# Performance work log

Hardware: AMD Instinct MI355X
Metric: run time of the kernel (lower is better)

Reference implementation:

```python
import jax, jax.numpy as jnp
import numpy as np

NEG_INF = -1e30  # stand-in for -inf that is safe under fp16/bf16


def setup_inputs() -> dict:
    key = jax.random.key(0)
    k1, k2, k3, k4, k5 = jax.random.split(key, 5)
    B, NC, H, Wd = 32, 256, 64, 64
    MW, E = 32, 768
    images = jax.random.normal(k1, (B, NC, H, Wd), dtype=jnp.float32)
    words = jax.random.normal(k2, (B, MW, E), dtype=jnp.float32)
    # mask: True where word is ignored; ensure at least one word is attended per row
    mask = jax.random.randint(k3, (B, MW), 0, 2).astype(bool)
    mask = mask.at[:, 0].set(False)
    W = jax.random.normal(k4, (NC, E), dtype=jnp.float32) * (1.0 / np.sqrt(E))
    b = jax.random.normal(k5, (NC,), dtype=jnp.float32) * 0.01
    return {"images": images, "words": words, "mask": mask, "W": W, "b": b}


def reference(images, words, mask, W, b):
    B, NC, H, Wd = images.shape
    _, MW, E = words.shape
    # 1x1 conv over words == linear projection emb_dim -> nc_in
    # words_p: [B, nc_in, max_words]
    words_p = jnp.einsum('bme,ce->bcm', words, W) + b[None, :, None]
    # images flattened to pixels: [B, h*w, nc_in]
    imgs = images.reshape(B, NC, H * Wd).transpose(0, 2, 1)
    # attention scores: [B, h*w, max_words], scaled by 1/sqrt(nc_in)
    attn = jnp.einsum('bpc,bcm->bpm', imgs, words_p) * (1.0 / np.sqrt(NC))
    attn = jnp.where(mask[:, None, :], NEG_INF, attn)
    attn = jax.nn.softmax(attn, axis=-1)
    # weighted word sum per pixel: [B, nc_in, h*w]
    weighted = jnp.einsum('bcm,bpm->bcp', words_p, attn)
    weighted_words = weighted.reshape(B, NC, H, Wd)
    attn_out = attn.transpose(0, 2, 1).reshape(B, MW, H, Wd)
    return weighted_words, attn_out
```

## Files before the change

kernel.cpp:

```cpp
#include <hip/hip_runtime.h>
#include <math.h>

#define B_   32
#define NC_  256
#define HW_  4096
#define MW_  32
#define E_   768
#define NEG_BIG -3.0e38f

typedef float vf2 __attribute__((ext_vector_type(2)));
typedef float vf4 __attribute__((ext_vector_type(4)));

#define PART_OFF   0
#define WP_OFF     2097152
#define WT_OFF     2359296
#define WORDST_OFF 2555904
#define MASK_OFF   3342336

__global__ __launch_bounds__(256) void prep_kernel(
    const float* __restrict__ W, const float* __restrict__ words,
    const void* __restrict__ mask_raw,
    float* __restrict__ WT, float* __restrict__ wordsT,
    int* __restrict__ maskn) {
  const int tid = threadIdx.x;
  const int tx = tid & 31, ty = tid >> 5;
  if (blockIdx.x < 192) {
    __shared__ float t[32][33];
    const int tc = blockIdx.x / 24, te = blockIdx.x % 24;
    const int c0 = tc * 32, e0 = te * 32;
#pragma unroll
    for (int k = 0; k < 4; ++k) {
      const int r = ty + 8 * k;
      t[r][tx] = W[(c0 + r) * E_ + e0 + tx];
    }
    __syncthreads();
#pragma unroll
    for (int k = 0; k < 4; ++k) {
      const int r = ty + 8 * k;
      WT[(e0 + r) * NC_ + c0 + tx] = t[tx][r];
    }
  } else if (blockIdx.x < 960) {
    __shared__ float t[32][33];
    const int idx = blockIdx.x - 192;
    const int b = idx / 24, te = idx % 24;
    const int e0 = te * 32;
    const float* wsrc = words + (size_t)b * MW_ * E_;
    float* wdst = wordsT + (size_t)b * E_ * MW_;
#pragma unroll
    for (int k = 0; k < 4; ++k) {
      const int m = ty + 8 * k;
      t[m][tx] = wsrc[m * E_ + e0 + tx];
    }
    __syncthreads();
#pragma unroll
    for (int k = 0; k < 4; ++k) {
      const int e = ty + 8 * k;
      wdst[(e0 + e) * MW_ + tx] = t[tx][e];
    }
  } else {
    __shared__ int is_word;
    if (tid == 0) is_word = 1;
    __syncthreads();
    const int* mi = (const int*)mask_raw;
    const int v = mi[tid];
    if (v != 0 && v != 1 && v != 0x3F800000) is_word = 0;
    __syncthreads();
    if (is_word) {
#pragma unroll
      for (int j = 0; j < 4; ++j) { const int i = j * 256 + tid; maskn[i] = (mi[i] != 0); }
    } else {
      const unsigned char* mb = (const unsigned char*)mask_raw;
#pragma unroll
      for (int j = 0; j < 4; ++j) { const int i = j * 256 + tid; maskn[i] = (mb[i] != 0); }
    }
  }
}

__global__ __launch_bounds__(256) void stage1_partial(
    const float* __restrict__ wordsT, const float* __restrict__ WT,
    float* __restrict__ part) {
  const int c = threadIdx.x;
  const int b = blockIdx.x >> 3;
  const int chunk = blockIdx.x & 7;
  const int e0 = chunk * 96;
  const float* wt = wordsT + (size_t)b * E_ * MW_;
  float acc[32];
#pragma unroll
  for (int m = 0; m < 32; ++m) acc[m] = 0.f;
#pragma unroll 2
  for (int e = e0; e < e0 + 96; ++e) {
    const float wv = WT[(size_t)e * NC_ + c];
    const float* wr = wt + e * MW_;
#pragma unroll
    for (int m = 0; m < 32; ++m) acc[m] = fmaf(wv, wr[m], acc[m]);
  }
  float* pp = part + ((size_t)chunk * 32 + b) * 32 * 256;
#pragma unroll
  for (int m = 0; m < 32; ++m) pp[m * 256 + c] = acc[m];
}

__global__ __launch_bounds__(256) void stage1_reduce(
    const float* __restrict__ part, const float* __restrict__ bias,
    float* __restrict__ wp) {
  const int idx = blockIdx.x * 256 + threadIdx.x;
  const int c = idx & 255;
  const int m = (idx >> 8) & 31;
  const int b = idx >> 13;
  float s = bias[c];
#pragma unroll
  for (int k = 0; k < 8; ++k)
    s += part[(((size_t)k * 32 + b) * 32 + m) * 256 + c];
  wp[((size_t)b * 256 + c) * 32 + m] = s;
}

__global__ __launch_bounds__(128, 1) void attention_fused(
    const float* __restrict__ images, const float* __restrict__ wp,
    const int* __restrict__ maskn, float* __restrict__ out_w,
    float* __restrict__ out_a) {
  __shared__ float lwp[NC_ * MW_];
  const int tid = threadIdx.x;
  const int b = blockIdx.x & 31;
  const int po = ((blockIdx.x >> 5) << 7) + tid;
  const vf2* imgb = (const vf2*)(images + (size_t)b * NC_ * HW_);

  vf2 cur[16];
#pragma unroll
  for (int j = 0; j < 16; ++j)
    cur[j] = __builtin_nontemporal_load(&imgb[((size_t)j << 11) + po]);

  {
    const vf4* src = (const vf4*)(wp + (size_t)b * NC_ * MW_);
    vf4* dst = (vf4*)lwp;
#pragma unroll
    for (int k = 0; k < 16; ++k) dst[tid + (k << 7)] = src[tid + (k << 7)];
  }
  __syncthreads();

  float s0[32], s1[32];
#pragma unroll
  for (int m = 0; m < 32; ++m) { s0[m] = 0.f; s1[m] = 0.f; }

#pragma unroll 1
  for (int c0 = 0; c0 < 256; c0 += 16) {
    vf2 nxt[16];
    if (c0 + 16 < 256) {
#pragma unroll
      for (int j = 0; j < 16; ++j)
        nxt[j] = __builtin_nontemporal_load(&imgb[((size_t)(c0 + 16 + j) << 11) + po]);
    }
#pragma unroll
    for (int j = 0; j < 16; ++j) {
      const float* wrow = lwp + ((c0 + j) << 5);
      const vf2 v = cur[j];
#pragma unroll
      for (int m = 0; m < 32; ++m) {
        s0[m] = fmaf(v.x, wrow[m], s0[m]);
        s1[m] = fmaf(v.y, wrow[m], s1[m]);
      }
    }
#pragma unroll
    for (int j = 0; j < 16; ++j) cur[j] = nxt[j];
  }

  unsigned mbits = 0;
#pragma unroll
  for (int m = 0; m < 32; ++m)
    mbits |= (maskn[(b << 5) + m] != 0 ? 1u : 0u) << m;

  float mx0 = NEG_BIG, mx1 = NEG_BIG;
#pragma unroll
  for (int m = 0; m < 32; ++m) {
    s0[m] *= 0.0625f;
    s1[m] *= 0.0625f;
    if (!((mbits >> m) & 1u)) {
      mx0 = fmaxf(mx0, s0[m]);
      mx1 = fmaxf(mx1, s1[m]);
    }
  }
  float sum0 = 0.f, sum1 = 0.f;
#pragma unroll
  for (int m = 0; m < 32; ++m) {
    const bool msk = (mbits >> m) & 1u;
    const float e0 = msk ? 0.f : __expf(s0[m] - mx0);
    const float e1 = msk ? 0.f : __expf(s1[m] - mx1);
    s0[m] = e0; s1[m] = e1;
    sum0 += e0; sum1 += e1;
  }
  const float inv0 = 1.f / sum0, inv1 = 1.f / sum1;
  vf2* oa = (vf2*)out_a;
#pragma unroll
  for (int m = 0; m < 32; ++m) {
    s0[m] *= inv0;
    s1[m] *= inv1;
    vf2 a; a.x = s0[m]; a.y = s1[m];
    __builtin_nontemporal_store(a, &oa[((size_t)((b << 5) + m) << 11) + po]);
  }

  vf2* ow = (vf2*)out_w;
#pragma unroll 1
  for (int c0 = 0; c0 < 256; c0 += 8) {
#pragma unroll
    for (int jc = 0; jc < 8; ++jc) {
      const int c = c0 + jc;
      const float* wrow = lwp + (c << 5);
      float o0 = 0.f, o1 = 0.f;
#pragma unroll
      for (int m = 0; m < 32; ++m) {
        o0 = fmaf(wrow[m], s0[m], o0);
        o1 = fmaf(wrow[m], s1[m], o1);
      }
      vf2 o; o.x = o0; o.y = o1;
      __builtin_nontemporal_store(o, &ow[((size_t)((b << 8) + c) << 11) + po]);
    }
  }
}

extern "C" void kernel_launch(void* const* d_in, const int* in_sizes, int n_in,
                              void* d_out, int out_size, void* d_ws, size_t ws_size,
                              hipStream_t stream) {
  const float* images = (const float*)d_in[0];
  const float* words  = (const float*)d_in[1];
  const void*  mask   = d_in[2];
  const float* W      = (const float*)d_in[3];
  const float* bias   = (const float*)d_in[4];

  float* ws     = (float*)d_ws;
  float* part   = ws + PART_OFF;
  float* wp     = ws + WP_OFF;
  float* WT     = ws + WT_OFF;
  float* wordsT = ws + WORDST_OFF;
  int*   maskn  = (int*)(ws + MASK_OFF);

  float* out_w = (float*)d_out;
  float* out_a = out_w + (size_t)B_ * NC_ * HW_;

  prep_kernel<<<961, 256, 0, stream>>>(W, words, mask, WT, wordsT, maskn);
  stage1_partial<<<256, 256, 0, stream>>>(wordsT, WT, part);
  stage1_reduce<<<1024, 256, 0, stream>>>(part, bias, wp);
  attention_fused<<<512, 128, 0, stream>>>(images, wp, maskn, out_w, out_a);
}
```

Measured before the change: 308.3 us.

## Fuse stage1 reduction and mask decoding into attention kernel, double-buffer weight rows

Removes the stage1_reduce kernel and the mask-normalization block: each attention block now sums the 8 partial projections plus bias directly into shared memory and decodes the mask bits itself. The image prefetch depth drops from 16 to 8 channels, launch bounds no longer force 1 block per SM, and weight rows are double-buffered from LDS into registers for both GEMM loops. This saves a kernel launch and a global round-trip for wp, but every one of the 512 blocks now redundantly re-reduces the partials (16x duplicated reads per batch) and register pressure changes.

```diff
diff --git a/kernel.cpp b/kernel.cpp
--- a/kernel.cpp
+++ b/kernel.cpp
@@ -12,16 +12,12 @@
 typedef float vf4 __attribute__((ext_vector_type(4)));
 
 #define PART_OFF   0
-#define WP_OFF     2097152
 #define WT_OFF     2359296
 #define WORDST_OFF 2555904
-#define MASK_OFF   3342336
 
 __global__ __launch_bounds__(256) void prep_kernel(
     const float* __restrict__ W, const float* __restrict__ words,
-    const void* __restrict__ mask_raw,
-    float* __restrict__ WT, float* __restrict__ wordsT,
-    int* __restrict__ maskn) {
+    float* __restrict__ WT, float* __restrict__ wordsT) {
   const int tid = threadIdx.x;
   const int tx = tid & 31, ty = tid >> 5;
   if (blockIdx.x < 192) {
@@ -39,7 +35,7 @@
       const int r = ty + 8 * k;
       WT[(e0 + r) * NC_ + c0 + tx] = t[tx][r];
     }
-  } else if (blockIdx.x < 960) {
+  } else {
     __shared__ float t[32][33];
     const int idx = blockIdx.x - 192;
     const int b = idx / 24, te = idx % 24;
@@ -56,22 +52,6 @@
     for (int k = 0; k < 4; ++k) {
       const int e = ty + 8 * k;
       wdst[(e0 + e) * MW_ + tx] = t[tx][e];
-    }
-  } else {
-    __shared__ int is_word;
-    if (tid == 0) is_word = 1;
-    __syncthreads();
-    const int* mi = (const int*)mask_raw;
-    const int v = mi[tid];
-    if (v != 0 && v != 1 && v != 0x3F800000) is_word = 0;
-    __syncthreads();
-    if (is_word) {
-#pragma unroll
-      for (int j = 0; j < 4; ++j) { const int i = j * 256 + tid; maskn[i] = (mi[i] != 0); }
-    } else {
-      const unsigned char* mb = (const unsigned char*)mask_raw;
-#pragma unroll
-      for (int j = 0; j < 4; ++j) { const int i = j * 256 + tid; maskn[i] = (mb[i] != 0); }
     }
   }
 }
@@ -99,73 +79,118 @@
   for (int m = 0; m < 32; ++m) pp[m * 256 + c] = acc[m];
 }
 
-__global__ __launch_bounds__(256) void stage1_reduce(
-    const float* __restrict__ part, const float* __restrict__ bias,
-    float* __restrict__ wp) {
-  const int idx = blockIdx.x * 256 + threadIdx.x;
-  const int c = idx & 255;
-  const int m = (idx >> 8) & 31;
-  const int b = idx >> 13;
-  float s = bias[c];
-#pragma unroll
-  for (int k = 0; k < 8; ++k)
-    s += part[(((size_t)k * 32 + b) * 32 + m) * 256 + c];
-  wp[((size_t)b * 256 + c) * 32 + m] = s;
-}
-
-__global__ __launch_bounds__(128, 1) void attention_fused(
-    const float* __restrict__ images, const float* __restrict__ wp,
-    const int* __restrict__ maskn, float* __restrict__ out_w,
-    float* __restrict__ out_a) {
+__global__ __launch_bounds__(128) void attention_fused(
+    const float* __restrict__ images, const float* __restrict__ part,
+    const float* __restrict__ bias, const void* __restrict__ mask_raw,
+    float* __restrict__ out_w, float* __restrict__ out_a) {
   __shared__ float lwp[NC_ * MW_];
+  __shared__ int is_word;
   const int tid = threadIdx.x;
   const int b = blockIdx.x & 31;
   const int po = ((blockIdx.x >> 5) << 7) + tid;
   const vf2* imgb = (const vf2*)(images + (size_t)b * NC_ * HW_);
 
-  vf2 cur[16];
-#pragma unroll
-  for (int j = 0; j < 16; ++j)
+  if (tid == 0) is_word = 1;
+
+  vf2 cur[8];
+#pragma unroll
+  for (int j = 0; j < 8; ++j)
     cur[j] = __builtin_nontemporal_load(&imgb[((size_t)j << 11) + po]);
 
+#pragma unroll
+  for (int half = 0; half < 2; ++half) {
+    const int c = (half << 7) + tid;
+    const float bc = bias[c];
+    float row[32];
+#pragma unroll
+    for (int m = 0; m < 32; ++m) row[m] = bc;
+#pragma unroll
+    for (int k = 0; k < 8; ++k) {
+      const float* pk = part + (((size_t)k * 32 + b) * 32) * 256 + c;
+#pragma unroll
+      for (int m = 0; m < 32; ++m) row[m] += pk[(size_t)m * 256];
+    }
+    vf4* dst = (vf4*)(lwp + (c << 5));
+#pragma unroll
+    for (int q = 0; q < 8; ++q) {
+      vf4 t;
+      t.x = row[4 * q]; t.y = row[4 * q + 1];
+      t.z = row[4 * q + 2]; t.w = row[4 * q + 3];
+      dst[q] = t;
+    }
+  }
+  __syncthreads();
+
   {
-    const vf4* src = (const vf4*)(wp + (size_t)b * NC_ * MW_);
-    vf4* dst = (vf4*)lwp;
-#pragma unroll
-    for (int k = 0; k < 16; ++k) dst[tid + (k << 7)] = src[tid + (k << 7)];
+    const int* mi = (const int*)mask_raw;
+#pragma unroll
+    for (int q = 0; q < 2; ++q) {
+      const int v = mi[q * 128 + tid];
+      if (v != 0 && v != 1 && v != 0x3F800000) is_word = 0;
+    }
   }
   __syncthreads();
+  unsigned mbits = 0;
+  if (is_word) {
+    const int* mi = (const int*)mask_raw;
+#pragma unroll
+    for (int m = 0; m < 32; ++m)
+      mbits |= (mi[(b << 5) + m] != 0 ? 1u : 0u) << m;
+  } else {
+    const unsigned char* mb = (const unsigned char*)mask_raw;
+#pragma unroll
+    for (int m = 0; m < 32; ++m)
+      mbits |= (mb[(b << 5) + m] != 0 ? 1u : 0u) << m;
+  }
 
   float s0[32], s1[32];
 #pragma unroll
   for (int m = 0; m < 32; ++m) { s0[m] = 0.f; s1[m] = 0.f; }
 
+  vf4 wa[8], wb[8];
+#pragma unroll
+  for (int q = 0; q < 8; ++q) wa[q] = ((const vf4*)lwp)[q];
+
 #pragma unroll 1
-  for (int c0 = 0; c0 < 256; c0 += 16) {
-    vf2 nxt[16];
-    if (c0 + 16 < 256) {
-#pragma unroll
-      for (int j = 0; j < 16; ++j)
-        nxt[j] = __builtin_nontemporal_load(&imgb[((size_t)(c0 + 16 + j) << 11) + po]);
-    }
-#pragma unroll
-    for (int j = 0; j < 16; ++j) {
-      const float* wrow = lwp + ((c0 + j) << 5);
-      const vf2 v = cur[j];
-#pragma unroll
-      for (int m = 0; m < 32; ++m) {
-        s0[m] = fmaf(v.x, wrow[m], s0[m]);
-        s1[m] = fmaf(v.y, wrow[m], s1[m]);
+  for (int c0 = 0; c0 < 256; c0 += 8) {
+    vf2 nxt[8];
+    if (c0 + 8 < 256) {
+#pragma unroll
+      for (int j = 0; j < 8; ++j)
+        nxt[j] = __builtin_nontemporal_load(&imgb[((size_t)(c0 + 8 + j) << 11) + po]);
+    }
+#pragma unroll
+    for (int j = 0; j < 8; ++j) {
+      const int cn = c0 + j + 1;
+      if ((j & 1) == 0) {
+        if (cn < 256) {
+#pragma unroll
+          for (int q = 0; q < 8; ++q) wb[q] = ((const vf4*)lwp)[(cn << 3) + q];
+        }
+        const float* wr = (const float*)wa;
+        const vf2 v = cur[j];
+#pragma unroll
+        for (int m = 0; m < 32; ++m) {
+          s0[m] = fmaf(v.x, wr[m], s0[m]);
+          s1[m] = fmaf(v.y, wr[m], s1[m]);
+        }
+      } else {
+        if (cn < 256) {
+#pragma unroll
+          for (int q = 0; q < 8; ++q) wa[q] = ((const vf4*)lwp)[(cn << 3) + q];
+        }
+        const float* wr = (const float*)wb;
+        const vf2 v = cur[j];
+#pragma unroll
+        for (int m = 0; m < 32; ++m) {
+          s0[m] = fmaf(v.x, wr[m], s0[m]);
+          s1[m] = fmaf(v.y, wr[m], s1[m]);
+        }
       }
     }
 #pragma unroll
-    for (int j = 0; j < 16; ++j) cur[j] = nxt[j];
-  }
-
-  unsigned mbits = 0;
-#pragma unroll
-  for (int m = 0; m < 32; ++m)
-    mbits |= (maskn[(b << 5) + m] != 0 ? 1u : 0u) << m;
+    for (int j = 0; j < 8; ++j) cur[j] = nxt[j];
+  }
 
   float mx0 = NEG_BIG, mx1 = NEG_BIG;
 #pragma unroll
@@ -197,17 +222,38 @@
   }
 
   vf2* ow = (vf2*)out_w;
+#pragma unroll
+  for (int q = 0; q < 8; ++q) wa[q] = ((const vf4*)lwp)[q];
+
 #pragma unroll 1
   for (int c0 = 0; c0 < 256; c0 += 8) {
 #pragma unroll
-    for (int jc = 0; jc < 8; ++jc) {
-      const int c = c0 + jc;
-      const float* wrow = lwp + (c << 5);
+    for (int j = 0; j < 8; ++j) {
+      const int c = c0 + j;
+      const int cn = c + 1;
       float o0 = 0.f, o1 = 0.f;
-#pragma unroll
-      for (int m = 0; m < 32; ++m) {
-        o0 = fmaf(wrow[m], s0[m], o0);
-        o1 = fmaf(wrow[m], s1[m], o1);
+      if ((j & 1) == 0) {
+        if (cn < 256) {
+#pragma unroll
+          for (int q = 0; q < 8; ++q) wb[q] = ((const vf4*)lwp)[(cn << 3) + q];
+        }
+        const float* wr = (const float*)wa;
+#pragma unroll
+        for (int m = 0; m < 32; ++m) {
+          o0 = fmaf(wr[m], s0[m], o0);
+          o1 = fmaf(wr[m], s1[m], o1);
+        }
+      } else {
+        if (cn < 256) {
+#pragma unroll
+          for (int q = 0; q < 8; ++q) wa[q] = ((const vf4*)lwp)[(cn << 3) + q];
+        }
+        const float* wr = (const float*)wb;
+#pragma unroll
+        for (int m = 0; m < 32; ++m) {
+          o0 = fmaf(wr[m], s0[m], o0);
+          o1 = fmaf(wr[m], s1[m], o1);
+        }
       }
       vf2 o; o.x = o0; o.y = o1;
       __builtin_nontemporal_store(o, &ow[((size_t)((b << 8) + c) << 11) + po]);
@@ -226,16 +272,13 @@
 
   float* ws     = (float*)d_ws;
   float* part   = ws + PART_OFF;
-  float* wp     = ws + WP_OFF;
   float* WT     = ws + WT_OFF;
   float* wordsT = ws + WORDST_OFF;
-  int*   maskn  = (int*)(ws + MASK_OFF);
 
   float* out_w = (float*)d_out;
   float* out_a = out_w + (size_t)B_ * NC_ * HW_;
 
-  prep_kernel<<<961, 256, 0, stream>>>(W, words, mask, WT, wordsT, maskn);
+  prep_kernel<<<960, 256, 0, stream>>>(W, words, WT, wordsT);
   stage1_partial<<<256, 256, 0, stream>>>(wordsT, WT, part);
-  stage1_reduce<<<1024, 256, 0, stream>>>(part, bias, wp);
-  attention_fused<<<512, 128, 0, stream>>>(images, wp, maskn, out_w, out_a);
-}
+  attention_fused<<<512, 128, 0, stream>>>(images, part, bias, mask, out_w, out_a);
+}
```

Measured after the change: 318.6 us. 3.3% more time.
